# Optimization experiments

Measured on AMD Instinct MI355X. Metric: run time of the kernel, lower is better.

Reference implementation:

```python
import jax, jax.numpy as jnp
import numpy as np


def setup_inputs() -> dict:
    key = jax.random.key(0)
    k1, k2 = jax.random.split(key)
    B, C, L = 128, 3, 2048
    K, S = 128, 50
    x = jax.random.normal(k1, (B, C, L), dtype=jnp.float32)
    shapelets = jax.random.normal(k2, (C, K, S), dtype=jnp.float32)
    return {"x": x, "shapelets": shapelets}


def reference(x, shapelets):
    # x: (B, C, L); shapelets: (C, K, S)
    S = shapelets.shape[-1]
    L = x.shape[-1]
    W = L - S + 1  # num sliding windows, stride 1
    # unfold: (B, C, W, S)
    idx = jnp.arange(W)[:, None] + jnp.arange(S)[None, :]
    windows = x[:, :, idx]
    # euclidean cdist via ||a||^2 + ||b||^2 - 2 a.b (matches use_mm_for_euclid_dist)
    sq_w = jnp.sum(windows * windows, axis=-1)          # (B, C, W)
    sq_s = jnp.sum(shapelets * shapelets, axis=-1)      # (C, K)
    dots = jnp.einsum('bcws,cks->bcwk', windows, shapelets)  # (B, C, W, K)
    d2 = sq_w[..., None] + sq_s[None, :, None, :] - 2.0 * dots
    dist = jnp.sqrt(jnp.maximum(d2, 0.0))               # (B, C, W, K)
    # sum over channels (keepdim), min over windows
    summed = jnp.sum(dist, axis=1, keepdims=True)        # (B, 1, W, K)
    out = jnp.min(summed, axis=2)                        # (B, 1, K)
    return out
```

## Files before the change

kernel.cpp:

```cpp
#include <hip/hip_runtime.h>
#include <math.h>

#define B_  128
#define C_  3
#define L_  2048
#define K_  128
#define S_  50
#define W_  (L_ - S_ + 1)
#define XPAD 2112
#define BIGW 1e30f

typedef __attribute__((ext_vector_type(8))) short bf16x8;
typedef __attribute__((ext_vector_type(4))) float f32x4;
typedef uint4 uint4_a4 __attribute__((aligned(4)));

__device__ __forceinline__ unsigned short f2bf(float f) {
    unsigned int u = __float_as_uint(f);
    u += 0x7FFFu + ((u >> 16) & 1u);
    return (unsigned short)(u >> 16);
}
__device__ __forceinline__ float bf2f(unsigned short h) {
    return __uint_as_float(((unsigned int)h) << 16);
}
__device__ __forceinline__ unsigned pack2(float a, float b) {
    return (unsigned)f2bf(a) | ((unsigned)f2bf(b) << 16);
}
__device__ __forceinline__ unsigned packsw(float s) {
    unsigned short hi = f2bf(s);
    unsigned short lo = f2bf(s - bf2f(hi));
    return (unsigned)hi | ((unsigned)lo << 16);
}

#define WS_SQWZ_OFF 0
#define WS_XB0_OFF  3145728
#define WS_XB1_OFF  4767744
#define WS_FRAG_OFF 6389760

__global__ __launch_bounds__(256) void prep_all(const float* __restrict__ x,
                                                const float* __restrict__ sh,
                                                unsigned* __restrict__ sqwz,
                                                unsigned* __restrict__ xb0,
                                                unsigned* __restrict__ xb1,
                                                uint4* __restrict__ ws_frag,
                                                float* __restrict__ out) {
    const int blk = blockIdx.x;
    if (blk < 396) {
        int i   = blk * 256 + threadIdx.x;
        int row = i / 264;
        int wi  = (i - row * 264) << 2;
        int pos = wi << 1;
        const float* xr = x + row * L_;
        float e[9];
        if (pos <= 2032) {
            float4 a = *(const float4*)(xr + pos);
            float4 b = *(const float4*)(xr + pos + 4);
            e[0]=a.x; e[1]=a.y; e[2]=a.z; e[3]=a.w;
            e[4]=b.x; e[5]=b.y; e[6]=b.z; e[7]=b.w;
            e[8]=xr[pos + 8];
        } else {
            #pragma unroll
            for (int j = 0; j < 9; ++j) e[j] = (pos + j < L_) ? xr[pos + j] : 0.f;
        }
        uint4 q0, q1;
        q0.x = pack2(e[0], e[1]); q0.y = pack2(e[2], e[3]);
        q0.z = pack2(e[4], e[5]); q0.w = pack2(e[6], e[7]);
        q1.x = pack2(e[1], e[2]); q1.y = pack2(e[3], e[4]);
        q1.z = pack2(e[5], e[6]); q1.w = pack2(e[7], e[8]);
        *(uint4*)(xb0 + row * (XPAD / 2) + wi) = q0;
        *(uint4*)(xb1 + row * (XPAD / 2) + wi) = q1;
    } else if (blk < 780) {
        int t   = (blk - 396) * 256 + threadIdx.x;
        int row = t >> 8;
        int wb  = (t & 255) * 8;
        const float* xr = x + row * L_;
        unsigned* op = sqwz + row * L_ + wb;
        if (wb <= 1984) {
            float4 f[15];
            #pragma unroll
            for (int q = 0; q < 15; ++q) f[q] = *(const float4*)(xr + wb + q * 4);
            float e[60];
            #pragma unroll
            for (int q = 0; q < 15; ++q) {
                e[4*q]=f[q].x; e[4*q+1]=f[q].y; e[4*q+2]=f[q].z; e[4*q+3]=f[q].w;
            }
            float s = 0.f;
            #pragma unroll
            for (int j = 0; j < S_; ++j) s += e[j] * e[j];
            op[0] = packsw(s);
            #pragma unroll
            for (int w = 1; w < 8; ++w) {
                s += e[w + 49] * e[w + 49] - e[w - 1] * e[w - 1];
                op[w] = packsw(s);
            }
        } else {
            for (int w8 = 0; w8 < 8; ++w8) {
                int w = wb + w8;
                float r = BIGW;
                if (w < W_) {
                    r = 0.f;
                    #pragma unroll 10
                    for (int j = 0; j < S_; ++j) { float v = xr[w + j]; r += v * v; }
                }
                op[w8] = packsw(r);
            }
        }
    } else if (blk < 792) {
        int t  = (blk - 780) * 256 + threadIdx.x;
        int c  = t >> 10;
        int rem = t & 1023;
        int ks = rem >> 9;
        int nq = (rem >> 6) & 7;
        int l  = rem & 63;
        int k  = nq * 16 + (l & 15);
        int s0 = ks * 32 + (l >> 4) * 8;
        const float* sp = sh + (c * K_ + k) * S_;
        float ss = 0.f;
        #pragma unroll 10
        for (int s = 0; s < S_; ++s) { float v = sp[s]; ss += v * v; }
        unsigned short ss_hi = f2bf(ss);
        unsigned short ss_lo = f2bf(ss - bf2f(ss_hi));
        unsigned short h[8];
        #pragma unroll
        for (int j = 0; j < 8; ++j) {
            int s = s0 + j;
            unsigned short v;
            if      (s < S_)             v = f2bf(-2.f * sp[s]);
            else if (s == 50)            v = ss_hi;
            else if (s == 51)            v = ss_lo;
            else if (s == 52 || s == 53) v = 0x3F80;
            else                         v = 0;
            h[j] = v;
        }
        uint4 u;
        u.x = (unsigned)h[0] | ((unsigned)h[1] << 16);
        u.y = (unsigned)h[2] | ((unsigned)h[3] << 16);
        u.z = (unsigned)h[4] | ((unsigned)h[5] << 16);
        u.w = (unsigned)h[6] | ((unsigned)h[7] << 16);
        ws_frag[t] = u;
    } else {
        int i = (blk - 792) * 256 + threadIdx.x;
        out[i] = __int_as_float(0x7F800000);
    }
}

__global__ __launch_bounds__(512) void mfma_main(
        const unsigned* __restrict__ sqwz,
        const char* __restrict__ xb0,
        const char* __restrict__ xb1,
        const uint4* __restrict__ ws_frag,
        float* __restrict__ out) {
    const int b    = blockIdx.x >> 3;
    const int tile = blockIdx.x & 7;
    const int w0   = tile * 256;
    const int t    = threadIdx.x;
    const int wid  = t >> 6;
    const int l    = t & 63;
    const int row  = l & 15;
    const int kg   = l >> 4;
    const int wbase = w0 + wid * 32 + row;
    const int eb0   = wbase + kg * 8;

    __shared__ uint4 sF[3072];
    __shared__ float bmin[8][K_];

    #pragma unroll
    for (int j = 0; j < 6; ++j) sF[t + j * 512] = ws_frag[t + j * 512];

    const char* xbase = (wbase & 1) ? (xb1 + 2 * (eb0 - 1)) : (xb0 + 2 * eb0);
    const unsigned* szp = sqwz + b * C_ * L_ + wbase;

    uint4 A00[3], A10[3], A01[3], A11[3];
    #pragma unroll
    for (int c = 0; c < C_; ++c) {
        const char* xp = xbase + (b * C_ + c) * (XPAD * 2);
        A00[c] = *(const uint4_a4*)(xp);
        A10[c] = *(const uint4_a4*)(xp + 64);
        A01[c] = *(const uint4_a4*)(xp + 32);
        A11[c] = *(const uint4_a4*)(xp + 96);
        unsigned wz0 = szp[c * L_];
        unsigned wz1 = szp[c * L_ + 16];
        if (kg == 2) {
            A10[c].y = 0x3F803F80u; A10[c].z = wz0;
            A11[c].y = 0x3F803F80u; A11[c].z = wz1;
        }
    }
    __syncthreads();

    #pragma unroll
    for (int nq = 0; nq < 8; ++nq) {
        f32x4 ds0 = (f32x4){0.f, 0.f, 0.f, 0.f};
        f32x4 ds1 = (f32x4){0.f, 0.f, 0.f, 0.f};
        #pragma unroll
        for (int c = 0; c < C_; ++c) {
            uint4 b0 = sF[c * 1024 +       nq * 64 + l];
            uint4 b1 = sF[c * 1024 + 512 + nq * 64 + l];
            f32x4 z = (f32x4){0.f, 0.f, 0.f, 0.f};
            f32x4 acc0, acc1;
            acc0 = __builtin_amdgcn_mfma_f32_16x16x32_bf16(
                       __builtin_bit_cast(bf16x8, A00[c]), __builtin_bit_cast(bf16x8, b0), z, 0, 0, 0);
            acc1 = __builtin_amdgcn_mfma_f32_16x16x32_bf16(
                       __builtin_bit_cast(bf16x8, A01[c]), __builtin_bit_cast(bf16x8, b0), z, 0, 0, 0);
            acc0 = __builtin_amdgcn_mfma_f32_16x16x32_bf16(
                       __builtin_bit_cast(bf16x8, A10[c]), __builtin_bit_cast(bf16x8, b1), acc0, 0, 0, 0);
            acc1 = __builtin_amdgcn_mfma_f32_16x16x32_bf16(
                       __builtin_bit_cast(bf16x8, A11[c]), __builtin_bit_cast(bf16x8, b1), acc1, 0, 0, 0);
            #pragma unroll
            for (int r = 0; r < 4; ++r) {
                ds0[r] += __builtin_amdgcn_sqrtf(fmaxf(acc0[r], 0.f));
                ds1[r] += __builtin_amdgcn_sqrtf(fmaxf(acc1[r], 0.f));
            }
        }
        float m = fminf(fminf(ds0[0], ds0[1]), fminf(ds0[2], ds0[3]));
        float n = fminf(fminf(ds1[0], ds1[1]), fminf(ds1[2], ds1[3]));
        m = fminf(m, n);
        m = fminf(m, __shfl_xor(m, 16));
        m = fminf(m, __shfl_xor(m, 32));
        if (kg == 0) bmin[wid][nq * 16 + row] = m;
    }
    __syncthreads();
    if (t < K_) {
        float v = bmin[0][t];
        #pragma unroll
        for (int q = 1; q < 8; ++q) v = fminf(v, bmin[q][t]);
        atomicMin(reinterpret_cast<int*>(out) + b * K_ + t, __float_as_int(v));
    }
}

extern "C" void kernel_launch(void* const* d_in, const int* in_sizes, int n_in,
                              void* d_out, int out_size, void* d_ws, size_t ws_size,
                              hipStream_t stream) {
    const float* x  = (const float*)d_in[0];
    const float* sh = (const float*)d_in[1];
    float* out = (float*)d_out;

    unsigned* ws_sqwz = (unsigned*)((char*)d_ws + WS_SQWZ_OFF);
    unsigned* ws_xb0  = (unsigned*)((char*)d_ws + WS_XB0_OFF);
    unsigned* ws_xb1  = (unsigned*)((char*)d_ws + WS_XB1_OFF);
    uint4*    ws_frag = (uint4*)((char*)d_ws + WS_FRAG_OFF);

    prep_all<<<856, 256, 0, stream>>>(x, sh, ws_sqwz, ws_xb0, ws_xb1, ws_frag, out);
    mfma_main<<<128 * 8, 512, 0, stream>>>(
        ws_sqwz, (const char*)ws_xb0, (const char*)ws_xb1, ws_frag, out);
}
```

Measured before the change: 36.69 us.

## Split main kernel into smaller blocks over window tiles and shapelet halves

The MFMA kernel now launches four times as many blocks. Each block covers 128 windows and 64 shapelets instead of 256 windows and all 128, and each wave computes one 16-window tile instead of two. This halves shared memory and register arrays per block and adds a launch-bounds occupancy hint, aiming for better occupancy and load balance across CUs. In exchange, x fragments are reloaded across the two shapelet halves, there are more atomics, and there is more per-block setup. It also replaces fmax(·,0) with fabs before sqrt, which changes results only for negative rounding noise.

```diff
diff --git a/kernel.cpp b/kernel.cpp
--- a/kernel.cpp
+++ b/kernel.cpp
@@ -143,86 +143,83 @@
     }
 }
 
-__global__ __launch_bounds__(512) void mfma_main(
+__global__ __launch_bounds__(512, 8) void mfma_main(
         const unsigned* __restrict__ sqwz,
         const char* __restrict__ xb0,
         const char* __restrict__ xb1,
         const uint4* __restrict__ ws_frag,
         float* __restrict__ out) {
-    const int b    = blockIdx.x >> 3;
-    const int tile = blockIdx.x & 7;
-    const int w0   = tile * 256;
+    const int bid  = blockIdx.x;
+    const int half = bid & 1;
+    const int tile = (bid >> 1) & 15;
+    const int b    = bid >> 5;
     const int t    = threadIdx.x;
     const int wid  = t >> 6;
     const int l    = t & 63;
     const int row  = l & 15;
     const int kg   = l >> 4;
-    const int wbase = w0 + wid * 32 + row;
+    const int wbase = tile * 128 + wid * 16 + row;
     const int eb0   = wbase + kg * 8;
 
-    __shared__ uint4 sF[3072];
-    __shared__ float bmin[8][K_];
+    __shared__ uint4 sF[1536];
+    __shared__ float bmin[8][64];
 
     #pragma unroll
-    for (int j = 0; j < 6; ++j) sF[t + j * 512] = ws_frag[t + j * 512];
+    for (int j = 0; j < 3; ++j) {
+        int idx = j * 512 + t;
+        int c   = idx >> 9;
+        int r   = idx & 511;
+        int ks  = r >> 8;
+        int nql = (r >> 6) & 3;
+        int ll  = r & 63;
+        sF[idx] = ws_frag[c * 1024 + ks * 512 + (half * 4 + nql) * 64 + ll];
+    }
 
     const char* xbase = (wbase & 1) ? (xb1 + 2 * (eb0 - 1)) : (xb0 + 2 * eb0);
     const unsigned* szp = sqwz + b * C_ * L_ + wbase;
 
-    uint4 A00[3], A10[3], A01[3], A11[3];
+    uint4 A0[3], A1[3];
     #pragma unroll
     for (int c = 0; c < C_; ++c) {
         const char* xp = xbase + (b * C_ + c) * (XPAD * 2);
-        A00[c] = *(const uint4_a4*)(xp);
-        A10[c] = *(const uint4_a4*)(xp + 64);
-        A01[c] = *(const uint4_a4*)(xp + 32);
-        A11[c] = *(const uint4_a4*)(xp + 96);
-        unsigned wz0 = szp[c * L_];
-        unsigned wz1 = szp[c * L_ + 16];
+        A0[c] = *(const uint4_a4*)(xp);
+        A1[c] = *(const uint4_a4*)(xp + 64);
+        unsigned wz = szp[c * L_];
         if (kg == 2) {
-            A10[c].y = 0x3F803F80u; A10[c].z = wz0;
-            A11[c].y = 0x3F803F80u; A11[c].z = wz1;
+            A1[c].y = 0x3F803F80u; A1[c].z = wz;
         }
     }
     __syncthreads();
 
     #pragma unroll
-    for (int nq = 0; nq < 8; ++nq) {
-        f32x4 ds0 = (f32x4){0.f, 0.f, 0.f, 0.f};
-        f32x4 ds1 = (f32x4){0.f, 0.f, 0.f, 0.f};
+    for (int nql = 0; nql < 4; ++nql) {
+        f32x4 ds = (f32x4){0.f, 0.f, 0.f, 0.f};
         #pragma unroll
         for (int c = 0; c < C_; ++c) {
-            uint4 b0 = sF[c * 1024 +       nq * 64 + l];
-            uint4 b1 = sF[c * 1024 + 512 + nq * 64 + l];
+            uint4 b0 = sF[c * 512 +       nql * 64 + l];
+            uint4 b1 = sF[c * 512 + 256 + nql * 64 + l];
             f32x4 z = (f32x4){0.f, 0.f, 0.f, 0.f};
-            f32x4 acc0, acc1;
-            acc0 = __builtin_amdgcn_mfma_f32_16x16x32_bf16(
-                       __builtin_bit_cast(bf16x8, A00[c]), __builtin_bit_cast(bf16x8, b0), z, 0, 0, 0);
-            acc1 = __builtin_amdgcn_mfma_f32_16x16x32_bf16(
-                       __builtin_bit_cast(bf16x8, A01[c]), __builtin_bit_cast(bf16x8, b0), z, 0, 0, 0);
-            acc0 = __builtin_amdgcn_mfma_f32_16x16x32_bf16(
-                       __builtin_bit_cast(bf16x8, A10[c]), __builtin_bit_cast(bf16x8, b1), acc0, 0, 0, 0);
-            acc1 = __builtin_amdgcn_mfma_f32_16x16x32_bf16(
-                       __builtin_bit_cast(bf16x8, A11[c]), __builtin_bit_cast(bf16x8, b1), acc1, 0, 0, 0);
-            #pragma unroll
-            for (int r = 0; r < 4; ++r) {
-                ds0[r] += __builtin_amdgcn_sqrtf(fmaxf(acc0[r], 0.f));
-                ds1[r] += __builtin_amdgcn_sqrtf(fmaxf(acc1[r], 0.f));
-            }
-        }
-        float m = fminf(fminf(ds0[0], ds0[1]), fminf(ds0[2], ds0[3]));
-        float n = fminf(fminf(ds1[0], ds1[1]), fminf(ds1[2], ds1[3]));
-        m = fminf(m, n);
+            f32x4 acc;
+            acc = __builtin_amdgcn_mfma_f32_16x16x32_bf16(
+                      __builtin_bit_cast(bf16x8, A0[c]), __builtin_bit_cast(bf16x8, b0), z, 0, 0, 0);
+            acc = __builtin_amdgcn_mfma_f32_16x16x32_bf16(
+                      __builtin_bit_cast(bf16x8, A1[c]), __builtin_bit_cast(bf16x8, b1), acc, 0, 0, 0);
+            #pragma unroll
+            for (int r = 0; r < 4; ++r)
+                ds[r] += __builtin_amdgcn_sqrtf(__builtin_fabsf(acc[r]));
+        }
+        float m = fminf(fminf(ds[0], ds[1]), fminf(ds[2], ds[3]));
         m = fminf(m, __shfl_xor(m, 16));
         m = fminf(m, __shfl_xor(m, 32));
-        if (kg == 0) bmin[wid][nq * 16 + row] = m;
+        if (kg == 0) bmin[wid][nql * 16 + row] = m;
     }
     __syncthreads();
-    if (t < K_) {
+    if (t < 64) {
         float v = bmin[0][t];
         #pragma unroll
         for (int q = 1; q < 8; ++q) v = fminf(v, bmin[q][t]);
-        atomicMin(reinterpret_cast<int*>(out) + b * K_ + t, __float_as_int(v));
+        atomicMin(reinterpret_cast<int*>(out) + b * K_ + half * 64 + t,
+                  __float_as_int(v));
     }
 }
 
@@ -239,6 +236,6 @@
     uint4*    ws_frag = (uint4*)((char*)d_ws + WS_FRAG_OFF);
 
     prep_all<<<856, 256, 0, stream>>>(x, sh, ws_sqwz, ws_xb0, ws_xb1, ws_frag, out);
-    mfma_main<<<128 * 8, 512, 0, stream>>>(
+    mfma_main<<<128 * 16 * 2, 512, 0, stream>>>(
         ws_sqwz, (const char*)ws_xb0, (const char*)ws_xb1, ws_frag, out);
 }
```

Measured after the change: 36.69 us. About the same (+0.0%).
